# Performance work log

Measured on AMD Instinct MI355X. Metric: run time of the kernel, lower is better.

The kernel has to match this reference:

```python
import jax, jax.numpy as jnp
import numpy as np

B, T, I, H = 64, 512, 64, 512
D1, D2, O = 1024, 2048, 16384


def setup_inputs() -> dict:
    key = jax.random.key(0)
    ks = jax.random.split(key, 16)
    bnd = 1.0 / np.sqrt(H)

    def u(k, shape):
        return jax.random.uniform(k, shape, minval=-bnd, maxval=bnd, dtype=jnp.float32)

    inp = {
        "x": jax.random.normal(ks[0], (B, T, I), dtype=jnp.float32),
        "Wih0": u(ks[1], (4 * H, I)),
        "Whh0": u(ks[2], (4 * H, H)),
        "bih0": u(ks[3], (4 * H,)).at[H:2 * H].set(1.0),
        "bhh0": u(ks[4], (4 * H,)).at[H:2 * H].set(1.0),
        "Wih1": u(ks[5], (4 * H, H)),
        "Whh1": u(ks[6], (4 * H, H)),
        "bih1": u(ks[7], (4 * H,)).at[H:2 * H].set(1.0),
        "bhh1": u(ks[8], (4 * H,)).at[H:2 * H].set(1.0),
        "W1": jax.random.normal(ks[9], (D1, H), dtype=jnp.float32) * 0.05,
        "b1": jnp.zeros((D1,), jnp.float32),
        "W2": jax.random.normal(ks[10], (D2, D1), dtype=jnp.float32) * 0.03,
        "b2": jnp.zeros((D2,), jnp.float32),
        "W3": jax.random.normal(ks[11], (O, D2), dtype=jnp.float32) * 0.02,
        "b3": jnp.zeros((O,), jnp.float32),
    }
    return inp


def _cell(x_t, h, c, Wih, Whh, bih, bhh):
    # x_t: [B, in], h/c: [B, H]; gates: [B, 4H]
    gates = x_t @ Wih.T + h @ Whh.T + (bih + bhh)
    i, f, g, o = jnp.split(gates, 4, axis=-1)
    i = jax.nn.sigmoid(i)
    f = jax.nn.sigmoid(f)
    g = jnp.tanh(g)
    o = jax.nn.sigmoid(o)
    c_new = f * c + i * g
    h_new = o * jnp.tanh(c_new)
    return h_new, c_new


def reference(x, Wih0, Whh0, bih0, bhh0, Wih1, Whh1, bih1, bhh1,
              W1, b1, W2, b2, W3, b3):
    Bn = x.shape[0]
    z = jnp.zeros((Bn, H), x.dtype)
    xT = jnp.swapaxes(x, 0, 1)  # [T, B, I]

    def step(carry, x_t):
        h0, c0, h1, c1 = carry
        h0, c0 = _cell(x_t, h0, c0, Wih0, Whh0, bih0, bhh0)
        h1, c1 = _cell(h0, h1, c1, Wih1, Whh1, bih1, bhh1)
        return (h0, c0, h1, c1), None

    (h0, c0, h1, c1), _ = jax.lax.scan(step, (z, z, z, z), xT)
    # decoder MLP on final top-layer hidden state (== outputs[-1])
    y = jax.nn.relu(h1 @ W1.T + b1)
    y = jax.nn.relu(y @ W2.T + b2)
    return y @ W3.T + b3  # [B, O]
```

## Files before the change

### kernel.cpp

```cpp
#include <hip/hip_runtime.h>
#include <hip/hip_bf16.h>
#include <cstdio>


#define B_  64
#define T_  512
#define I_  64
#define H_  512
#define D1_ 1024
#define D2_ 2048
#define O_  16384

typedef __attribute__((ext_vector_type(8))) short bf16x8_t;
typedef __attribute__((ext_vector_type(4))) float f32x4_t;
typedef unsigned short ushort_t;

__device__ inline ushort_t f2bf(float f) {
    return __builtin_bit_cast(ushort_t, __float2bfloat16(f));
}
__device__ inline float sigm(float x) { return 1.0f / (1.0f + __expf(-x)); }
__device__ inline float tanhf_(float x) {
    float cx = fminf(fmaxf(x, -15.f), 15.f);
    float e = __expf(2.f * cx);
    return (e - 1.f) / (e + 1.f);
}


__global__ void pack_l0(const float* __restrict__ Wih0, const float* __restrict__ Whh0,
                        ushort_t* __restrict__ pack) {
    int idx = blockIdx.x * 256 + threadIdx.x;
    int l  = idx & 63;
    int kk = (idx >> 6) % 18;
    int tu = idx / (18 * 64);
    int jl = l & 15, g8 = (l >> 4) * 8;
    int gate = jl & 3, u = tu * 4 + (jl >> 2);
    int wrow = gate * H_ + u;
    int kg = kk * 32 + g8;
    const float* s = (kg < H_) ? (Whh0 + (size_t)wrow * H_ + kg)
                               : (Wih0 + (size_t)wrow * I_ + (kg - H_));
    ushort_t* d = pack + (size_t)idx * 8;
#pragma unroll
    for (int i = 0; i < 8; i++) d[i] = f2bf(s[i]);
}

__global__ void pack_l1(const float* __restrict__ Wih1, const float* __restrict__ Whh1,
                        ushort_t* __restrict__ pack) {
    int idx = blockIdx.x * 256 + threadIdx.x;
    int l  = idx & 63;
    int kk = (idx >> 6) & 31;
    int tu = idx >> 11;
    int jl = l & 15, g8 = (l >> 4) * 8;
    int gate = jl & 3, u = tu * 4 + (jl >> 2);
    int wrow = gate * H_ + u;
    int kg = kk * 32 + g8;
    const float* s = (kg < H_) ? (Wih1 + (size_t)wrow * H_ + kg)
                               : (Whh1 + (size_t)wrow * H_ + (kg - H_));
    ushort_t* d = pack + (size_t)idx * 8;
#pragma unroll
    for (int i = 0; i < 8; i++) d[i] = f2bf(s[i]);
}

__global__ void pack_bias(const float* __restrict__ bih0, const float* __restrict__ bhh0,
                          const float* __restrict__ bih1, const float* __restrict__ bhh1,
                          float* __restrict__ bsum) {
    int idx = blockIdx.x * 256 + threadIdx.x;
    int layer = idx >> 11;
    int rest = idx & 2047;
    int u = rest >> 2, gate = rest & 3;
    const float* a = layer ? bih1 : bih0;
    const float* b = layer ? bhh1 : bhh0;
    bsum[idx] = a[gate * H_ + u] + b[gate * H_ + u];
}

__global__ void conv_x(const float* __restrict__ x, ushort_t* __restrict__ xbf) {
    int idx = blockIdx.x * 256 + threadIdx.x;
    int c = idx & 63;
    int t = (idx >> 6) & 511;
    int b = idx >> 15;
    xbf[(size_t)t * 4096 + b * 64 + c] = f2bf(x[idx]);
}

__global__ __launch_bounds__(256) void lstm_step(
    int k,
    const ushort_t* __restrict__ packL0, const ushort_t* __restrict__ packL1,
    const float* __restrict__ bsum, const ushort_t* __restrict__ xbf,
    ushort_t* __restrict__ hbuf0, ushort_t* __restrict__ hbuf1,
    float* __restrict__ c0, float* __restrict__ c1)
{
    __shared__ uint4 aLDS4[2048];
    int w = blockIdx.x, tid = threadIdx.x;
    int l = tid & 63, v = tid >> 6;
    int layer = (w >= 128);
    int tu = layer ? (w - 128) : w;
    if (!layer && k >= T_) return;
    if (layer && k == 0) return;

    int nk = layer ? 32 : 18;
    const ushort_t* src = layer ? (packL1 + (size_t)tu * (32 * 512))
                                : (packL0 + (size_t)tu * (18 * 512));
    {
        const uint4* s4 = (const uint4*)src;
        for (int i = tid; i < nk * 64; i += 256) aLDS4[i] = s4[i];
    }
    __syncthreads();

    int u_loc = l >> 4;
    int bb = v * 16 + (l & 15);
    int u = tu * 4 + u_loc;
    const float* bp = bsum + layer * 2048 + u * 4;
    f32x4_t acc;
    acc[0] = bp[0]; acc[1] = bp[1]; acc[2] = bp[2]; acc[3] = bp[3];

    const int HS = 64 * 512;
    const ushort_t* h0r = hbuf0 + ((k + 1) & 1) * HS + bb * 512;
    const ushort_t* srcHi = layer ? (hbuf1 + (k & 1) * HS + bb * 512)
                                  : (xbf + (size_t)k * 4096 + bb * 64);
    int g8 = (l >> 4) * 8;

    const bf16x8_t* aF = (const bf16x8_t*)aLDS4;
    for (int kk = 0; kk < nk; ++kk) {
        bf16x8_t a = aF[kk * 64 + l];
        const ushort_t* bp_ = (kk < 16) ? (h0r + kk * 32 + g8)
                                        : (srcHi + (kk - 16) * 32 + g8);
        bf16x8_t b = *(const bf16x8_t*)bp_;
        acc = __builtin_amdgcn_mfma_f32_16x16x32_bf16(a, b, acc, 0, 0, 0);
    }

    float xi = sigm(acc[0]);
    float xf = sigm(acc[1]);
    float xg = tanhf_(acc[2]);
    float xo = sigm(acc[3]);
    float* cb = layer ? c1 : c0;
    size_t ci = (size_t)u * 64 + bb;
    float cn = xf * cb[ci] + xi * xg;
    cb[ci] = cn;
    float hn = xo * tanhf_(cn);
    ushort_t* hw = layer ? (hbuf1 + ((k + 1) & 1) * HS) : (hbuf0 + (k & 1) * HS);
    hw[(size_t)bb * 512 + u] = f2bf(hn);
}

template <int NK, bool RELU, bool OUTBF>
__global__ __launch_bounds__(256) void dec_gemm(
    const float* __restrict__ W, const float* __restrict__ bias,
    const ushort_t* __restrict__ act, void* __restrict__ outp, int ncols)
{
    int tile = blockIdx.x, tid = threadIdx.x;
    int l = tid & 63, v = tid >> 6;
    int bb = v * 16 + (l & 15);
    int jA = tile * 16 + (l & 15);
    int g8 = (l >> 4) * 8;
    const float* wrow = W + (size_t)jA * (NK * 32);
    const ushort_t* arow = act + (size_t)bb * (NK * 32);
    f32x4_t acc = {0.f, 0.f, 0.f, 0.f};
    for (int kk = 0; kk < NK; ++kk) {
        int kg = kk * 32 + g8;
        float4 w0 = *(const float4*)(wrow + kg);
        float4 w1 = *(const float4*)(wrow + kg + 4);
        bf16x8_t af;
        af[0] = (short)f2bf(w0.x); af[1] = (short)f2bf(w0.y);
        af[2] = (short)f2bf(w0.z); af[3] = (short)f2bf(w0.w);
        af[4] = (short)f2bf(w1.x); af[5] = (short)f2bf(w1.y);
        af[6] = (short)f2bf(w1.z); af[7] = (short)f2bf(w1.w);
        bf16x8_t bf = *(const bf16x8_t*)(arow + kg);
        acc = __builtin_amdgcn_mfma_f32_16x16x32_bf16(af, bf, acc, 0, 0, 0);
    }
    int j0 = tile * 16 + (l >> 4) * 4;
    float r[4];
#pragma unroll
    for (int i = 0; i < 4; i++) {
        r[i] = acc[i] + bias[j0 + i];
        if (RELU) r[i] = fmaxf(r[i], 0.f);
    }
    if (OUTBF) {
        ushort_t* o = (ushort_t*)outp + (size_t)bb * ncols + j0;
        unsigned int lo = (unsigned)f2bf(r[0]) | ((unsigned)f2bf(r[1]) << 16);
        unsigned int hi = (unsigned)f2bf(r[2]) | ((unsigned)f2bf(r[3]) << 16);
        uint2 q; q.x = lo; q.y = hi;
        *(uint2*)o = q;
    } else {
        float* o = (float*)outp + (size_t)bb * ncols + j0;
        float4 t4; t4.x = r[0]; t4.y = r[1]; t4.z = r[2]; t4.w = r[3];
        *(float4*)o = t4;
    }
}

extern "C" void kernel_launch(void* const* d_in, const int* in_sizes, int n_in,
                              void* d_out, int out_size, void* d_ws, size_t ws_size,
                              hipStream_t stream)
{
    const float* x    = (const float*)d_in[0];
    const float* Wih0 = (const float*)d_in[1];
    const float* Whh0 = (const float*)d_in[2];
    const float* bih0 = (const float*)d_in[3];
    const float* bhh0 = (const float*)d_in[4];
    const float* Wih1 = (const float*)d_in[5];
    const float* Whh1 = (const float*)d_in[6];
    const float* bih1 = (const float*)d_in[7];
    const float* bhh1 = (const float*)d_in[8];
    const float* W1   = (const float*)d_in[9];
    const float* b1   = (const float*)d_in[10];
    const float* W2   = (const float*)d_in[11];
    const float* b2   = (const float*)d_in[12];
    const float* W3   = (const float*)d_in[13];
    const float* b3   = (const float*)d_in[14];

    char* ws = (char*)d_ws;
    size_t off = 0;
    auto take = [&](size_t bytes) -> char* {
        char* p = ws + off;
        off = (off + bytes + 255) & ~(size_t)255;
        return p;
    };
    ushort_t* packL0 = (ushort_t*)take((size_t)128 * 18 * 64 * 8 * 2);
    ushort_t* packL1 = (ushort_t*)take((size_t)128 * 32 * 64 * 8 * 2);
    float*    bsum   = (float*)take(2 * 2048 * 4);
    ushort_t* xbf    = (ushort_t*)take((size_t)512 * 64 * 64 * 2);
    char* zbase = ws + off;
    ushort_t* hbuf0  = (ushort_t*)take(2 * 64 * 512 * 2);
    ushort_t* hbuf1  = (ushort_t*)take(2 * 64 * 512 * 2);
    float*    c0     = (float*)take(512 * 64 * 4);
    float*    c1     = (float*)take(512 * 64 * 4);
    size_t zbytes = (size_t)((ws + off) - zbase);
    ushort_t* y1 = (ushort_t*)take(64 * 1024 * 2);
    ushort_t* y2 = (ushort_t*)take(64 * 2048 * 2);
    if (off > ws_size) {
        fprintf(stderr, "kernel_launch: ws too small: need %zu have %zu\n", off, ws_size);
        return;
    }

    pack_l0<<<(128 * 18 * 64) / 256, 256, 0, stream>>>(Wih0, Whh0, packL0);
    pack_l1<<<(128 * 32 * 64) / 256, 256, 0, stream>>>(Wih1, Whh1, packL1);
    pack_bias<<<16, 256, 0, stream>>>(bih0, bhh0, bih1, bhh1, bsum);
    conv_x<<<(64 * 512 * 64) / 256, 256, 0, stream>>>(x, xbf);
    hipMemsetAsync(zbase, 0, zbytes, stream);

    for (int k = 0; k <= T_; ++k)
        lstm_step<<<256, 256, 0, stream>>>(k, packL0, packL1, bsum, xbf,
                                           hbuf0, hbuf1, c0, c1);

    const ushort_t* h1f = hbuf1 + 1 * (64 * 512);
    dec_gemm<16, true,  true ><<<  64, 256, 0, stream>>>(W1, b1, h1f, y1, D1_);
    dec_gemm<32, true,  true ><<< 128, 256, 0, stream>>>(W2, b2, y1, y2, D2_);
    dec_gemm<64, false, false><<<1024, 256, 0, stream>>>(W3, b3, y2, d_out, O_);
}
```

Measured before the change: 4.613 ms.

## Fuse per-timestep LSTM launches into one persistent kernel with grid barrier

Replaces the 513 separate lstm_step launches with a single persistent kernel of 256 blocks. The blocks synchronise between timesteps with an atomic-counter grid barrier. Weights are held in registers across all timesteps instead of being reloaded into LDS on every launch. The cell state now lives in a register rather than global memory, and two accumulators split the MFMA dependency chain. This removes launch overhead and repeated weight reloads, but it relies on all 256 blocks being co-resident and adds global-atomic barrier latency and register pressure.

```diff
diff --git a/kernel.cpp b/kernel.cpp
--- a/kernel.cpp
+++ b/kernel.cpp
@@ -80,63 +80,90 @@
     xbf[(size_t)t * 4096 + b * 64 + c] = f2bf(x[idx]);
 }
 
-__global__ __launch_bounds__(256) void lstm_step(
-    int k,
+
+__device__ inline void grid_barrier(unsigned int* cnt, int iter, int tid) {
+    __syncthreads();
+    if (tid == 0) {
+        __hip_atomic_fetch_add(cnt, 1u, __ATOMIC_RELEASE, __HIP_MEMORY_SCOPE_AGENT);
+        unsigned int target = 256u * (unsigned int)(iter + 1);
+        while (__hip_atomic_load(cnt, __ATOMIC_ACQUIRE, __HIP_MEMORY_SCOPE_AGENT) < target)
+            __builtin_amdgcn_s_sleep(1);
+    }
+    __syncthreads();
+}
+
+template <int LAYER>
+__device__ void run_layer(int tu, int tid,
+                          const ushort_t* __restrict__ pack,
+                          const float* __restrict__ bsum,
+                          const ushort_t* __restrict__ xbf,
+                          ushort_t* __restrict__ hbuf0,
+                          ushort_t* __restrict__ hbuf1,
+                          unsigned int* __restrict__ cnt)
+{
+    constexpr int NK = LAYER ? 32 : 18;
+    int l = tid & 63, v = tid >> 6;
+    int u_loc = l >> 4;
+    int bb = v * 16 + (l & 15);
+    int u = tu * 4 + u_loc;
+    int g8 = u_loc * 8;
+
+    bf16x8_t aF[NK];
+    {
+        const ushort_t* src = pack + (size_t)tu * (NK * 512) + l * 8;
+#pragma unroll
+        for (int kk = 0; kk < NK; ++kk)
+            aF[kk] = *(const bf16x8_t*)(src + kk * 512);
+    }
+    const float* bp = bsum + LAYER * 2048 + u * 4;
+    float bi0 = bp[0], bi1 = bp[1], bi2 = bp[2], bi3 = bp[3];
+    float creg = 0.0f;
+
+    const int HS = 64 * 512;
+    for (int k = 0; k <= T_; ++k) {
+        bool active = LAYER ? (k >= 1) : (k < T_);
+        if (active) {
+            const ushort_t* h0r = hbuf0 + ((k + 1) & 1) * HS + bb * 512;
+            const ushort_t* srcHi = LAYER ? (hbuf1 + (k & 1) * HS + bb * 512)
+                                          : (xbf + (size_t)k * 4096 + bb * 64);
+            f32x4_t acc  = {bi0, bi1, bi2, bi3};
+            f32x4_t acc2 = {0.f, 0.f, 0.f, 0.f};
+#pragma unroll
+            for (int kk = 0; kk < NK; ++kk) {
+                const ushort_t* q = (kk < 16) ? (h0r + kk * 32 + g8)
+                                              : (srcHi + (kk - 16) * 32 + g8);
+                bf16x8_t bfr = *(const bf16x8_t*)q;
+                if (kk & 1)
+                    acc2 = __builtin_amdgcn_mfma_f32_16x16x32_bf16(aF[kk], bfr, acc2, 0, 0, 0);
+                else
+                    acc  = __builtin_amdgcn_mfma_f32_16x16x32_bf16(aF[kk], bfr, acc, 0, 0, 0);
+            }
+            acc = acc + acc2;
+            float xi = sigm(acc[0]);
+            float xf = sigm(acc[1]);
+            float xg = tanhf_(acc[2]);
+            float xo = sigm(acc[3]);
+            creg = xf * creg + xi * xg;
+            float hn = xo * tanhf_(creg);
+            ushort_t* hw = LAYER ? (hbuf1 + ((k + 1) & 1) * HS)
+                                 : (hbuf0 + (k & 1) * HS);
+            hw[(size_t)bb * 512 + u] = f2bf(hn);
+        }
+        grid_barrier(cnt, k, tid);
+    }
+}
+
+__global__ __launch_bounds__(256) void lstm_persist(
     const ushort_t* __restrict__ packL0, const ushort_t* __restrict__ packL1,
     const float* __restrict__ bsum, const ushort_t* __restrict__ xbf,
     ushort_t* __restrict__ hbuf0, ushort_t* __restrict__ hbuf1,
-    float* __restrict__ c0, float* __restrict__ c1)
-{
-    __shared__ uint4 aLDS4[2048];
+    unsigned int* __restrict__ cnt)
+{
     int w = blockIdx.x, tid = threadIdx.x;
-    int l = tid & 63, v = tid >> 6;
-    int layer = (w >= 128);
-    int tu = layer ? (w - 128) : w;
-    if (!layer && k >= T_) return;
-    if (layer && k == 0) return;
-
-    int nk = layer ? 32 : 18;
-    const ushort_t* src = layer ? (packL1 + (size_t)tu * (32 * 512))
-                                : (packL0 + (size_t)tu * (18 * 512));
-    {
-        const uint4* s4 = (const uint4*)src;
-        for (int i = tid; i < nk * 64; i += 256) aLDS4[i] = s4[i];
-    }
-    __syncthreads();
-
-    int u_loc = l >> 4;
-    int bb = v * 16 + (l & 15);
-    int u = tu * 4 + u_loc;
-    const float* bp = bsum + layer * 2048 + u * 4;
-    f32x4_t acc;
-    acc[0] = bp[0]; acc[1] = bp[1]; acc[2] = bp[2]; acc[3] = bp[3];
-
-    const int HS = 64 * 512;
-    const ushort_t* h0r = hbuf0 + ((k + 1) & 1) * HS + bb * 512;
-    const ushort_t* srcHi = layer ? (hbuf1 + (k & 1) * HS + bb * 512)
-                                  : (xbf + (size_t)k * 4096 + bb * 64);
-    int g8 = (l >> 4) * 8;
-
-    const bf16x8_t* aF = (const bf16x8_t*)aLDS4;
-    for (int kk = 0; kk < nk; ++kk) {
-        bf16x8_t a = aF[kk * 64 + l];
-        const ushort_t* bp_ = (kk < 16) ? (h0r + kk * 32 + g8)
-                                        : (srcHi + (kk - 16) * 32 + g8);
-        bf16x8_t b = *(const bf16x8_t*)bp_;
-        acc = __builtin_amdgcn_mfma_f32_16x16x32_bf16(a, b, acc, 0, 0, 0);
-    }
-
-    float xi = sigm(acc[0]);
-    float xf = sigm(acc[1]);
-    float xg = tanhf_(acc[2]);
-    float xo = sigm(acc[3]);
-    float* cb = layer ? c1 : c0;
-    size_t ci = (size_t)u * 64 + bb;
-    float cn = xf * cb[ci] + xi * xg;
-    cb[ci] = cn;
-    float hn = xo * tanhf_(cn);
-    ushort_t* hw = layer ? (hbuf1 + ((k + 1) & 1) * HS) : (hbuf0 + (k & 1) * HS);
-    hw[(size_t)bb * 512 + u] = f2bf(hn);
+    if (w < 128)
+        run_layer<0>(w, tid, packL0, bsum, xbf, hbuf0, hbuf1, cnt);
+    else
+        run_layer<1>(w - 128, tid, packL1, bsum, xbf, hbuf0, hbuf1, cnt);
 }
 
 template <int NK, bool RELU, bool OUTBF>
@@ -218,8 +245,7 @@
     char* zbase = ws + off;
     ushort_t* hbuf0  = (ushort_t*)take(2 * 64 * 512 * 2);
     ushort_t* hbuf1  = (ushort_t*)take(2 * 64 * 512 * 2);
-    float*    c0     = (float*)take(512 * 64 * 4);
-    float*    c1     = (float*)take(512 * 64 * 4);
+    unsigned int* cnt = (unsigned int*)take(256);
     size_t zbytes = (size_t)((ws + off) - zbase);
     ushort_t* y1 = (ushort_t*)take(64 * 1024 * 2);
     ushort_t* y2 = (ushort_t*)take(64 * 2048 * 2);
@@ -234,9 +260,8 @@
     conv_x<<<(64 * 512 * 64) / 256, 256, 0, stream>>>(x, xbf);
     hipMemsetAsync(zbase, 0, zbytes, stream);
 
-    for (int k = 0; k <= T_; ++k)
-        lstm_step<<<256, 256, 0, stream>>>(k, packL0, packL1, bsum, xbf,
-                                           hbuf0, hbuf1, c0, c1);
+    lstm_persist<<<256, 256, 0, stream>>>(packL0, packL1, bsum, xbf,
+                                          hbuf0, hbuf1, cnt);
 
     const ushort_t* h1f = hbuf1 + 1 * (64 * 512);
     dec_gemm<16, true,  true ><<<  64, 256, 0, stream>>>(W1, b1, h1f, y1, D1_);
```

Result: slower. 11.81 ms (+156.1%).
